# Performance work log

Hardware: AMD Instinct MI355X
Metric: run time of the kernel (lower is better)

The kernel has to match this reference:

```python
import jax, jax.numpy as jnp
import numpy as np

B, T, F, D, K, C, O = 256, 16, 8, 32, 64, 1024, 2

def setup_inputs():
    ks = jax.random.split(jax.random.key(0), 16)
    return {
        "tdata": jax.random.normal(ks[0], (B, T, F, D), jnp.float32),
        "f_mask": jax.random.randint(ks[1], (B, T, F), 0, 2, jnp.int32),
        "centers": jax.random.normal(ks[2], (F, K, D), jnp.float32),
        "pat": jax.random.randint(ks[3], (F, C, F), 0, K + 2, jnp.int32),
        "pat_rep": jax.random.normal(ks[4], (F, C, D), jnp.float32),
        "pos_cnt": jax.random.uniform(ks[5], (F, C), jnp.float32),
        "neg_cnt": jax.random.uniform(ks[6], (F, C), jnp.float32),
        "W_q": jax.random.normal(ks[7], (F, D, D), jnp.float32) * 0.1,
        "b_q": jax.random.normal(ks[8], (F, D), jnp.float32) * 0.1,
        "W_k": jax.random.normal(ks[9], (F, D, D + 1), jnp.float32) * 0.1,
        "b_k": jax.random.normal(ks[10], (F, D), jnp.float32) * 0.1,
        "W_v": jax.random.normal(ks[11], (F, D + 1, D + 1), jnp.float32) * 0.1,
        "b_v": jax.random.normal(ks[12], (F, D + 1), jnp.float32) * 0.1,
        "W_pred": jax.random.normal(ks[13], (O, F * (D + 1)), jnp.float32) * 0.1,
    }

def reference(tdata, f_mask, centers, pat, pat_rep, pos_cnt, neg_cnt,
              W_q, b_q, W_k, b_k, W_v, b_v, W_pred):
    Bv, Tv, Fv, Dv = tdata.shape
    BT = Bv * Tv
    fdata = tdata.reshape(BT, Fv, Dv)                     # [BT, F, D]

    # --- VQ nearest-centroid codes per feature (compute_codes) ---
    def codes_one(x, cen):                                # x [BT, D], cen [K, D]
        d = (jnp.sum(x * x, 1, keepdims=True)
             - 2.0 * (x @ cen.T)
             + jnp.sum(cen * cen, 1)[None, :])
        return jnp.argmin(d, axis=1)
    codes = jax.vmap(codes_one, in_axes=(1, 0), out_axes=1)(fdata, centers)  # [BT, F]
    mflat = f_mask.reshape(BT, Fv)
    # scatter_add equivalent: masked positions get code+2, unmasked get 1
    f_codes = jnp.where(mflat != 0, codes.astype(jnp.int32) + 2, 1)          # [BT, F]

    ratio = pos_cnt / (pos_cnt + neg_cnt + 1e-6)          # [F, C]
    rep = jnp.concatenate([pat_rep, ratio[..., None]], axis=-1)  # [F, C, D+1]
    query = tdata[:, -1]                                  # [B, F, D]

    def per_feature(pat_i, rep_i, q_i, Wq, bq, Wk, bk, Wv, bv):
        # pattern match: wildcard (0) always matches, else code must equal
        wild = pat_i == 0                                 # [C, F]
        eq = jnp.where(wild[None], True, f_codes[:, None, :] == pat_i[None])  # [BT, C, F]
        match = jnp.any(jnp.all(eq, axis=2).reshape(Bv, Tv, -1), axis=1)      # [B, C]
        key_t = match[..., None].astype(rep_i.dtype) * rep_i[None]            # [B, C, D+1]
        iq = q_i @ Wq.T + bq                              # [B, D]
        ik = key_t @ Wk.T + bk                            # [B, C, D]
        iv = key_t @ Wv.T + bv                            # [B, C, D+1]
        e = jnp.einsum('bcd,bd->bc', ik, iq)
        e = e - (1.0 - match.astype(e.dtype)) * 1e7
        a = jax.nn.softmax(e, axis=-1)
        v = jnp.einsum('bc,bcd->bd', a, iv)               # [B, D+1]
        return v, a

    v_all, a_all = jax.vmap(per_feature, in_axes=(0, 0, 1, 0, 0, 0, 0, 0, 0))(
        pat, rep, query, W_q, b_q, W_k, b_k, W_v, b_v)    # [F,B,D+1], [F,B,C]
    srep = jnp.swapaxes(v_all, 0, 1)                      # [B, F, D+1]
    fm = jnp.any(f_mask != 0, axis=1).astype(srep.dtype)  # [B, F]
    srep = srep * fm[..., None]
    cali = srep.reshape(Bv, -1) @ W_pred.T                # [B, O]
    return cali, a_all, srep
```

## Files before the change

### kernel.cpp

```cpp
#include <hip/hip_runtime.h>
#include <math.h>

#define Bv 256
#define Tv 16
#define Fv 8
#define Dv 32
#define Kv 64
#define Cv 1024
#define Ov 2
#define D1 33
#define CSTRIDE 33

typedef unsigned long long u64;
typedef unsigned char u8;

struct SM {
  float cen[4 * Kv * CSTRIDE];
  float xsh[Tv * Fv * Dv];
  u64   cds[Tv];
  int   fmask[Tv * Fv];
  int   fm_arr[Fv];
  int   anyf[Fv][4];
  float srep_all[Fv * D1];
  float iqs[Dv], zs[D1 + 1], vsum[D1];
  float redm[4], reds[4];
};

__device__ __forceinline__ void codes_pass(SM& sm, int pass,
    const float* __restrict__ centers) {
  int tid = threadIdx.x;
  int w = tid >> 6, lane = tid & 63;
  const float4* src = (const float4*)(centers + pass * 4 * Kv * Dv);
  #pragma unroll
  for (int it = 0; it < 8; it++) {
    int g4 = tid + it * 256;
    float4 v = src[g4];
    int g = g4 * 4;
    int row = g >> 5, col = g & 31;
    float* dst = &sm.cen[row * CSTRIDE + col];
    dst[0] = v.x; dst[1] = v.y; dst[2] = v.z; dst[3] = v.w;
  }
  __syncthreads();
  int ff = pass * 4 + w;
  float crow[Dv];
  float cc = 0.f;
  const float* rowp = &sm.cen[(w * Kv + lane) * CSTRIDE];
  #pragma unroll
  for (int j = 0; j < Dv; j++) { float cv = rowp[j]; crow[j] = cv; cc += cv * cv; }
  for (int t = 0; t < Tv; t++) {
    const float4* xp = (const float4*)&sm.xsh[(t * Fv + ff) * Dv];
    float dot = 0.f;
    #pragma unroll
    for (int i = 0; i < 8; i++) {
      float4 xv = xp[i];
      dot += crow[i*4+0]*xv.x + crow[i*4+1]*xv.y + crow[i*4+2]*xv.z + crow[i*4+3]*xv.w;
    }
    float bd = cc - 2.0f * dot;
    int bk = lane;
    #pragma unroll
    for (int off = 32; off >= 1; off >>= 1) {
      float od = __shfl_xor(bd, off, 64);
      int ok = __shfl_xor(bk, off, 64);
      if (od < bd || (od == bd && ok < bk)) { bd = od; bk = ok; }
    }
    if (lane == 0) {
      int m = sm.fmask[t * Fv + ff];
      ((u8*)sm.cds)[t * Fv + ff] = (u8)(m != 0 ? bk + 2 : 1);
    }
  }
  __syncthreads();
}

__global__ __launch_bounds__(256) void fused(
    const float* __restrict__ tdata, const int* __restrict__ f_mask,
    const float* __restrict__ centers, const int* __restrict__ pat,
    const float* __restrict__ pat_rep, const float* __restrict__ pos_cnt,
    const float* __restrict__ neg_cnt,
    const float* __restrict__ W_q, const float* __restrict__ b_q,
    const float* __restrict__ W_k, const float* __restrict__ b_k,
    const float* __restrict__ W_v, const float* __restrict__ b_v,
    const float* __restrict__ W_pred,
    float* __restrict__ cali, float* __restrict__ a_out,
    float* __restrict__ srep_out) {
  __shared__ SM sm;
  int b = blockIdx.x, tid = threadIdx.x;

  {
    const float4* src = (const float4*)(tdata + (size_t)b * (Tv * Fv * Dv));
    float4* dst = (float4*)sm.xsh;
    #pragma unroll
    for (int it = 0; it < 4; it++) dst[tid + it * 256] = src[tid + it * 256];
    if (tid < Tv * Fv) sm.fmask[tid] = f_mask[b * (Tv * Fv) + tid];
  }
  codes_pass(sm, 0, centers);
  if (tid < Fv) {
    int a = 0;
    #pragma unroll
    for (int t = 0; t < Tv; t++) a |= sm.fmask[t * Fv + tid];
    sm.fm_arr[tid] = (a != 0);
  }
  codes_pass(sm, 1, centers);

  u64 creg[Tv];
  #pragma unroll
  for (int t = 0; t < Tv; t++) creg[t] = sm.cds[t];

  for (int f = 0; f < Fv; f++) {
    u64 pp[4], cm[4];
    bool mt[4];
    #pragma unroll
    for (int jj = 0; jj < 4; jj++) {
      int c = tid + (jj << 8);
      const int4* pr = (const int4*)(pat + ((size_t)f * Cv + c) * Fv);
      int4 pa = pr[0], pb = pr[1];
      int vals[8] = {pa.x, pa.y, pa.z, pa.w, pb.x, pb.y, pb.z, pb.w};
      u64 P = 0, M = 0;
      #pragma unroll
      for (int k = 0; k < 8; k++) {
        P |= ((u64)(vals[k] & 0xFF)) << (8 * k);
        if (vals[k] != 0) M |= 0xFFull << (8 * k);
      }
      pp[jj] = P; cm[jj] = M;
      bool m = false;
      #pragma unroll
      for (int t = 0; t < Tv; t++) m = m || (((creg[t] ^ P) & M) == 0ull);
      mt[jj] = m;
    }
    bool lany = mt[0] || mt[1] || mt[2] || mt[3];
    bool wv = __any((int)lany);
    if ((tid & 63) == 0) sm.anyf[f][tid >> 6] = wv ? 1 : 0;
    __syncthreads();
    bool anym = (sm.anyf[f][0] | sm.anyf[f][1] | sm.anyf[f][2] | sm.anyf[f][3]) != 0;
    bool fm = sm.fm_arr[f] != 0;
    float* arow = a_out + (size_t)(f * Bv + b) * Cv;

    if (!anym) {
      const float uu = 1.0f / 1024.0f;
      #pragma unroll
      for (int jj = 0; jj < 4; jj++) arow[tid + (jj << 8)] = uu;
      if (tid < D1) {
        float vd = fm ? b_v[f * D1 + tid] : 0.f;
        sm.srep_all[f * D1 + tid] = vd;
        srep_out[(b * Fv + f) * D1 + tid] = vd;
      }
      continue;
    }

    if (tid < D1) sm.vsum[tid] = 0.f;
    __syncthreads();
    if (tid < Dv) {
      const float* xq = &sm.xsh[((Tv - 1) * Fv + f) * Dv];
      const float* wq = W_q + (f * Dv + tid) * Dv;
      float s = b_q[f * Dv + tid];
      #pragma unroll
      for (int j = 0; j < Dv; j++) s += wq[j] * xq[j];
      sm.iqs[tid] = s;
    }
    __syncthreads();
    if (tid < D1) {
      float s = 0.f;
      #pragma unroll
      for (int i = 0; i < Dv; i++) s += W_k[(f * Dv + i) * D1 + tid] * sm.iqs[i];
      sm.zs[tid] = s;
    }
    if (tid == D1) {
      float s = 0.f;
      #pragma unroll
      for (int i = 0; i < Dv; i++) s += b_k[f * Dv + i] * sm.iqs[i];
      sm.zs[D1] = s;
    }
    __syncthreads();

    float ev[4];
    float lmax = -INFINITY;
    #pragma unroll
    for (int jj = 0; jj < 4; jj++) {
      ev[jj] = 0.f;
      if (mt[jj]) {
        int c = tid + (jj << 8);
        const float* rp = pat_rep + (size_t)(f * Cv + c) * Dv;
        float p = pos_cnt[f * Cv + c], n = neg_cnt[f * Cv + c];
        float r = p / (p + n + 1e-6f);
        float s = sm.zs[D1] + r * sm.zs[Dv];
        for (int j = 0; j < Dv; j++) s += rp[j] * sm.zs[j];
        ev[jj] = s;
        lmax = fmaxf(lmax, s);
      }
    }
    float mx = lmax;
    #pragma unroll
    for (int off = 32; off >= 1; off >>= 1) mx = fmaxf(mx, __shfl_xor(mx, off, 64));
    if ((tid & 63) == 0) sm.redm[tid >> 6] = mx;
    __syncthreads();
    float bmax = fmaxf(fmaxf(sm.redm[0], sm.redm[1]), fmaxf(sm.redm[2], sm.redm[3]));

    float av[4] = {0.f, 0.f, 0.f, 0.f};
    float ls = 0.f;
    #pragma unroll
    for (int jj = 0; jj < 4; jj++) {
      if (mt[jj]) { av[jj] = expf(ev[jj] - bmax); ls += av[jj]; }
    }
    float ss = ls;
    #pragma unroll
    for (int off = 32; off >= 1; off >>= 1) ss += __shfl_xor(ss, off, 64);
    if ((tid & 63) == 0) sm.reds[tid >> 6] = ss;
    __syncthreads();
    float Z = sm.reds[0] + sm.reds[1] + sm.reds[2] + sm.reds[3];

    #pragma unroll
    for (int jj = 0; jj < 4; jj++) {
      float a = av[jj] / Z;
      arow[tid + (jj << 8)] = a;
      if (mt[jj] && av[jj] != 0.f) {
        int c = tid + (jj << 8);
        const float* rp = pat_rep + (size_t)(f * Cv + c) * Dv;
        float p = pos_cnt[f * Cv + c], n = neg_cnt[f * Cv + c];
        float r = p / (p + n + 1e-6f);
        for (int j = 0; j < Dv; j++) atomicAdd(&sm.vsum[j], a * rp[j]);
        atomicAdd(&sm.vsum[Dv], a * r);
      }
    }
    __syncthreads();
    float vreg = 0.f;
    if (tid < D1) {
      float s = b_v[f * D1 + tid];
      const float* wvp = W_v + (f * D1 + tid) * D1;
      for (int j = 0; j < D1; j++) s += wvp[j] * sm.vsum[j];
      vreg = s;
    }
    __syncthreads();
    if (tid < D1) {
      float vd = fm ? vreg : 0.f;
      sm.srep_all[f * D1 + tid] = vd;
      srep_out[(b * Fv + f) * D1 + tid] = vd;
    }
  }

  __syncthreads();
  if (tid < 64) {
    int o = tid >> 5, l = tid & 31;
    const float* wp = W_pred + o * (Fv * D1);
    float acc = 0.f;
    for (int i = l; i < Fv * D1; i += 32) acc += sm.srep_all[i] * wp[i];
    #pragma unroll
    for (int off = 16; off >= 1; off >>= 1) acc += __shfl_xor(acc, off, 64);
    if (l == 0) cali[b * Ov + o] = acc;
  }
}

extern "C" void kernel_launch(void* const* d_in, const int* in_sizes, int n_in,
                              void* d_out, int out_size, void* d_ws, size_t ws_size,
                              hipStream_t stream) {
  const float* tdata   = (const float*)d_in[0];
  const int*   f_mask  = (const int*)d_in[1];
  const float* centers = (const float*)d_in[2];
  const int*   pat     = (const int*)d_in[3];
  const float* pat_rep = (const float*)d_in[4];
  const float* pos_cnt = (const float*)d_in[5];
  const float* neg_cnt = (const float*)d_in[6];
  const float* W_q     = (const float*)d_in[7];
  const float* b_q     = (const float*)d_in[8];
  const float* W_k     = (const float*)d_in[9];
  const float* b_k     = (const float*)d_in[10];
  const float* W_v     = (const float*)d_in[11];
  const float* b_v     = (const float*)d_in[12];
  const float* W_pred  = (const float*)d_in[13];

  float* out = (float*)d_out;
  float* cali = out;
  float* a_all = out + (Bv * Ov);
  float* srep = out + (Bv * Ov) + (Fv * (size_t)Bv * Cv);

  fused<<<Bv, 256, 0, stream>>>(
      tdata, f_mask, centers, pat, pat_rep, pos_cnt, neg_cnt,
      W_q, b_q, W_k, b_k, W_v, b_v, W_pred,
      cali, a_all, srep);
}
```

Before: 124.6 us.

## Assign one wavefront per feature with 512 threads, removing block-wide barriers

```diff
diff --git a/kernel.cpp b/kernel.cpp
--- a/kernel.cpp
+++ b/kernel.cpp
@@ -9,69 +9,19 @@
 #define Cv 1024
 #define Ov 2
 #define D1 33
-#define CSTRIDE 33
 
 typedef unsigned long long u64;
 typedef unsigned char u8;
 
 struct SM {
-  float cen[4 * Kv * CSTRIDE];
   float xsh[Tv * Fv * Dv];
   u64   cds[Tv];
   int   fmask[Tv * Fv];
-  int   fm_arr[Fv];
-  int   anyf[Fv][4];
   float srep_all[Fv * D1];
-  float iqs[Dv], zs[D1 + 1], vsum[D1];
-  float redm[4], reds[4];
+  float vsum[Fv][D1];
 };
 
-__device__ __forceinline__ void codes_pass(SM& sm, int pass,
-    const float* __restrict__ centers) {
-  int tid = threadIdx.x;
-  int w = tid >> 6, lane = tid & 63;
-  const float4* src = (const float4*)(centers + pass * 4 * Kv * Dv);
-  #pragma unroll
-  for (int it = 0; it < 8; it++) {
-    int g4 = tid + it * 256;
-    float4 v = src[g4];
-    int g = g4 * 4;
-    int row = g >> 5, col = g & 31;
-    float* dst = &sm.cen[row * CSTRIDE + col];
-    dst[0] = v.x; dst[1] = v.y; dst[2] = v.z; dst[3] = v.w;
-  }
-  __syncthreads();
-  int ff = pass * 4 + w;
-  float crow[Dv];
-  float cc = 0.f;
-  const float* rowp = &sm.cen[(w * Kv + lane) * CSTRIDE];
-  #pragma unroll
-  for (int j = 0; j < Dv; j++) { float cv = rowp[j]; crow[j] = cv; cc += cv * cv; }
-  for (int t = 0; t < Tv; t++) {
-    const float4* xp = (const float4*)&sm.xsh[(t * Fv + ff) * Dv];
-    float dot = 0.f;
-    #pragma unroll
-    for (int i = 0; i < 8; i++) {
-      float4 xv = xp[i];
-      dot += crow[i*4+0]*xv.x + crow[i*4+1]*xv.y + crow[i*4+2]*xv.z + crow[i*4+3]*xv.w;
-    }
-    float bd = cc - 2.0f * dot;
-    int bk = lane;
-    #pragma unroll
-    for (int off = 32; off >= 1; off >>= 1) {
-      float od = __shfl_xor(bd, off, 64);
-      int ok = __shfl_xor(bk, off, 64);
-      if (od < bd || (od == bd && ok < bk)) { bd = od; bk = ok; }
-    }
-    if (lane == 0) {
-      int m = sm.fmask[t * Fv + ff];
-      ((u8*)sm.cds)[t * Fv + ff] = (u8)(m != 0 ? bk + 2 : 1);
-    }
-  }
-  __syncthreads();
-}
-
-__global__ __launch_bounds__(256) void fused(
+__global__ __launch_bounds__(512) void fused(
     const float* __restrict__ tdata, const int* __restrict__ f_mask,
     const float* __restrict__ centers, const int* __restrict__ pat,
     const float* __restrict__ pat_rep, const float* __restrict__ pos_cnt,
@@ -84,155 +34,161 @@
     float* __restrict__ srep_out) {
   __shared__ SM sm;
   int b = blockIdx.x, tid = threadIdx.x;
+  int w = tid >> 6, lane = tid & 63;
 
   {
     const float4* src = (const float4*)(tdata + (size_t)b * (Tv * Fv * Dv));
     float4* dst = (float4*)sm.xsh;
-    #pragma unroll
-    for (int it = 0; it < 4; it++) dst[tid + it * 256] = src[tid + it * 256];
+    dst[tid] = src[tid];
+    dst[tid + 512] = src[tid + 512];
     if (tid < Tv * Fv) sm.fmask[tid] = f_mask[b * (Tv * Fv) + tid];
   }
-  codes_pass(sm, 0, centers);
-  if (tid < Fv) {
-    int a = 0;
-    #pragma unroll
-    for (int t = 0; t < Tv; t++) a |= sm.fmask[t * Fv + tid];
-    sm.fm_arr[tid] = (a != 0);
-  }
-  codes_pass(sm, 1, centers);
-
+  __syncthreads();
+
+  {
+    const float4* cp = (const float4*)(centers + (size_t)(w * Kv + lane) * Dv);
+    float4 c4[8];
+    float cc = 0.f;
+    #pragma unroll
+    for (int i = 0; i < 8; i++) {
+      float4 v = cp[i];
+      c4[i] = v;
+      cc += v.x * v.x + v.y * v.y + v.z * v.z + v.w * v.w;
+    }
+    #pragma unroll
+    for (int t = 0; t < Tv; t += 2) {
+      const float4* x0 = (const float4*)&sm.xsh[(t * Fv + w) * Dv];
+      const float4* x1 = (const float4*)&sm.xsh[((t + 1) * Fv + w) * Dv];
+      float dot0 = 0.f, dot1 = 0.f;
+      #pragma unroll
+      for (int i = 0; i < 8; i++) {
+        float4 a = x0[i], bq = x1[i];
+        dot0 += c4[i].x * a.x + c4[i].y * a.y + c4[i].z * a.z + c4[i].w * a.w;
+        dot1 += c4[i].x * bq.x + c4[i].y * bq.y + c4[i].z * bq.z + c4[i].w * bq.w;
+      }
+      float d0 = cc - 2.0f * dot0;
+      float d1 = cc - 2.0f * dot1;
+      float m0 = d0, m1 = d1;
+      #pragma unroll
+      for (int off = 1; off <= 32; off <<= 1) {
+        m0 = fminf(m0, __shfl_xor(m0, off, 64));
+        m1 = fminf(m1, __shfl_xor(m1, off, 64));
+      }
+      u64 bl0 = __ballot(d0 == m0);
+      u64 bl1 = __ballot(d1 == m1);
+      int k0 = __ffsll(bl0) - 1;
+      int k1 = __ffsll(bl1) - 1;
+      if (lane == 0) {
+        ((u8*)sm.cds)[t * Fv + w] = sm.fmask[t * Fv + w] ? (u8)(k0 + 2) : (u8)1;
+        ((u8*)sm.cds)[(t + 1) * Fv + w] = sm.fmask[(t + 1) * Fv + w] ? (u8)(k1 + 2) : (u8)1;
+      }
+    }
+  }
+  __syncthreads();
+
+  int f = w;
   u64 creg[Tv];
   #pragma unroll
   for (int t = 0; t < Tv; t++) creg[t] = sm.cds[t];
 
-  for (int f = 0; f < Fv; f++) {
-    u64 pp[4], cm[4];
-    bool mt[4];
-    #pragma unroll
-    for (int jj = 0; jj < 4; jj++) {
-      int c = tid + (jj << 8);
-      const int4* pr = (const int4*)(pat + ((size_t)f * Cv + c) * Fv);
-      int4 pa = pr[0], pb = pr[1];
-      int vals[8] = {pa.x, pa.y, pa.z, pa.w, pb.x, pb.y, pb.z, pb.w};
-      u64 P = 0, M = 0;
-      #pragma unroll
-      for (int k = 0; k < 8; k++) {
-        P |= ((u64)(vals[k] & 0xFF)) << (8 * k);
-        if (vals[k] != 0) M |= 0xFFull << (8 * k);
-      }
-      pp[jj] = P; cm[jj] = M;
-      bool m = false;
-      #pragma unroll
-      for (int t = 0; t < Tv; t++) m = m || (((creg[t] ^ P) & M) == 0ull);
-      mt[jj] = m;
-    }
-    bool lany = mt[0] || mt[1] || mt[2] || mt[3];
-    bool wv = __any((int)lany);
-    if ((tid & 63) == 0) sm.anyf[f][tid >> 6] = wv ? 1 : 0;
-    __syncthreads();
-    bool anym = (sm.anyf[f][0] | sm.anyf[f][1] | sm.anyf[f][2] | sm.anyf[f][3]) != 0;
-    bool fm = sm.fm_arr[f] != 0;
-    float* arow = a_out + (size_t)(f * Bv + b) * Cv;
-
-    if (!anym) {
-      const float uu = 1.0f / 1024.0f;
-      #pragma unroll
-      for (int jj = 0; jj < 4; jj++) arow[tid + (jj << 8)] = uu;
-      if (tid < D1) {
-        float vd = fm ? b_v[f * D1 + tid] : 0.f;
-        sm.srep_all[f * D1 + tid] = vd;
-        srep_out[(b * Fv + f) * D1 + tid] = vd;
-      }
-      continue;
-    }
-
-    if (tid < D1) sm.vsum[tid] = 0.f;
-    __syncthreads();
-    if (tid < Dv) {
+  int fmlv = (lane < Tv) ? sm.fmask[lane * Fv + f] : 0;
+  bool fm = __any(fmlv != 0);
+
+  unsigned mask16 = 0u;
+  #pragma unroll 4
+  for (int jj = 0; jj < 16; jj++) {
+    int c = (jj << 6) + lane;
+    const int4* pr = (const int4*)(pat + ((size_t)f * Cv + c) * Fv);
+    int4 pa = pr[0], pb = pr[1];
+    int vals[8] = {pa.x, pa.y, pa.z, pa.w, pb.x, pb.y, pb.z, pb.w};
+    u64 P = 0, M = 0;
+    #pragma unroll
+    for (int k = 0; k < 8; k++) {
+      P |= ((u64)(vals[k] & 0xFF)) << (8 * k);
+      if (vals[k] != 0) M |= 0xFFull << (8 * k);
+    }
+    u64 pm = P & M;
+    bool m = false;
+    #pragma unroll
+    for (int t = 0; t < Tv; t++) m = m || ((creg[t] & M) == pm);
+    if (m) mask16 |= (1u << jj);
+  }
+  bool anym = __any(mask16 != 0u);
+
+  float* arow = a_out + (size_t)(f * Bv + b) * Cv;
+
+  if (!anym) {
+    const float uu = 1.0f / 1024.0f;
+    #pragma unroll
+    for (int jj = 0; jj < 16; jj++) arow[(jj << 6) + lane] = uu;
+    if (lane < D1) {
+      float vd = fm ? b_v[f * D1 + lane] : 0.f;
+      srep_out[(b * Fv + f) * D1 + lane] = vd;
+      sm.srep_all[f * D1 + lane] = vd;
+    }
+  } else {
+    if (lane < D1) sm.vsum[f][lane] = 0.f;
+    float iqv = 0.f;
+    if (lane < Dv) {
+      const float* wq = W_q + (f * Dv + lane) * Dv;
       const float* xq = &sm.xsh[((Tv - 1) * Fv + f) * Dv];
-      const float* wq = W_q + (f * Dv + tid) * Dv;
-      float s = b_q[f * Dv + tid];
-      #pragma unroll
+      float s = b_q[f * Dv + lane];
       for (int j = 0; j < Dv; j++) s += wq[j] * xq[j];
-      sm.iqs[tid] = s;
-    }
-    __syncthreads();
-    if (tid < D1) {
-      float s = 0.f;
-      #pragma unroll
-      for (int i = 0; i < Dv; i++) s += W_k[(f * Dv + i) * D1 + tid] * sm.iqs[i];
-      sm.zs[tid] = s;
-    }
-    if (tid == D1) {
-      float s = 0.f;
-      #pragma unroll
-      for (int i = 0; i < Dv; i++) s += b_k[f * Dv + i] * sm.iqs[i];
-      sm.zs[D1] = s;
-    }
-    __syncthreads();
-
-    float ev[4];
+      iqv = s;
+    }
+    float zv = 0.f;
+    for (int i = 0; i < Dv; i++) {
+      float iqi = __shfl(iqv, i, 64);
+      float coef = 0.f;
+      if (lane < D1) coef = W_k[(f * Dv + i) * D1 + lane];
+      else if (lane == D1) coef = b_k[f * Dv + i];
+      zv += coef * iqi;
+    }
+    float ev[16];
     float lmax = -INFINITY;
-    #pragma unroll
-    for (int jj = 0; jj < 4; jj++) {
+    for (int jj = 0; jj < 16; jj++) {
       ev[jj] = 0.f;
-      if (mt[jj]) {
-        int c = tid + (jj << 8);
-        const float* rp = pat_rep + (size_t)(f * Cv + c) * Dv;
+      if (mask16 & (1u << jj)) {
+        int c = (jj << 6) + lane;
+        const float* rp = pat_rep + ((size_t)f * Cv + c) * Dv;
         float p = pos_cnt[f * Cv + c], n = neg_cnt[f * Cv + c];
         float r = p / (p + n + 1e-6f);
-        float s = sm.zs[D1] + r * sm.zs[Dv];
-        for (int j = 0; j < Dv; j++) s += rp[j] * sm.zs[j];
+        float s = __shfl(zv, D1, 64) + r * __shfl(zv, Dv, 64);
+        for (int j = 0; j < Dv; j++) s += rp[j] * __shfl(zv, j, 64);
         ev[jj] = s;
         lmax = fmaxf(lmax, s);
       }
     }
-    float mx = lmax;
-    #pragma unroll
-    for (int off = 32; off >= 1; off >>= 1) mx = fmaxf(mx, __shfl_xor(mx, off, 64));
-    if ((tid & 63) == 0) sm.redm[tid >> 6] = mx;
-    __syncthreads();
-    float bmax = fmaxf(fmaxf(sm.redm[0], sm.redm[1]), fmaxf(sm.redm[2], sm.redm[3]));
-
-    float av[4] = {0.f, 0.f, 0.f, 0.f};
+    float bm = lmax;
+    #pragma unroll
+    for (int off = 1; off <= 32; off <<= 1) bm = fmaxf(bm, __shfl_xor(bm, off, 64));
     float ls = 0.f;
-    #pragma unroll
-    for (int jj = 0; jj < 4; jj++) {
-      if (mt[jj]) { av[jj] = expf(ev[jj] - bmax); ls += av[jj]; }
-    }
-    float ss = ls;
-    #pragma unroll
-    for (int off = 32; off >= 1; off >>= 1) ss += __shfl_xor(ss, off, 64);
-    if ((tid & 63) == 0) sm.reds[tid >> 6] = ss;
-    __syncthreads();
-    float Z = sm.reds[0] + sm.reds[1] + sm.reds[2] + sm.reds[3];
-
-    #pragma unroll
-    for (int jj = 0; jj < 4; jj++) {
-      float a = av[jj] / Z;
-      arow[tid + (jj << 8)] = a;
-      if (mt[jj] && av[jj] != 0.f) {
-        int c = tid + (jj << 8);
-        const float* rp = pat_rep + (size_t)(f * Cv + c) * Dv;
+    for (int jj = 0; jj < 16; jj++) {
+      if (mask16 & (1u << jj)) { ev[jj] = expf(ev[jj] - bm); ls += ev[jj]; }
+    }
+    float Zs = ls;
+    #pragma unroll
+    for (int off = 1; off <= 32; off <<= 1) Zs += __shfl_xor(Zs, off, 64);
+    for (int jj = 0; jj < 16; jj++) {
+      int c = (jj << 6) + lane;
+      bool hit = (mask16 & (1u << jj)) != 0u;
+      float a = hit ? ev[jj] / Zs : 0.f;
+      arow[c] = a;
+      if (hit && a != 0.f) {
+        const float* rp = pat_rep + ((size_t)f * Cv + c) * Dv;
         float p = pos_cnt[f * Cv + c], n = neg_cnt[f * Cv + c];
         float r = p / (p + n + 1e-6f);
-        for (int j = 0; j < Dv; j++) atomicAdd(&sm.vsum[j], a * rp[j]);
-        atomicAdd(&sm.vsum[Dv], a * r);
-      }
-    }
-    __syncthreads();
-    float vreg = 0.f;
-    if (tid < D1) {
-      float s = b_v[f * D1 + tid];
-      const float* wvp = W_v + (f * D1 + tid) * D1;
-      for (int j = 0; j < D1; j++) s += wvp[j] * sm.vsum[j];
-      vreg = s;
-    }
-    __syncthreads();
-    if (tid < D1) {
-      float vd = fm ? vreg : 0.f;
-      sm.srep_all[f * D1 + tid] = vd;
-      srep_out[(b * Fv + f) * D1 + tid] = vd;
+        for (int j = 0; j < Dv; j++) atomicAdd(&sm.vsum[f][j], a * rp[j]);
+        atomicAdd(&sm.vsum[f][Dv], a * r);
+      }
+    }
+    if (lane < D1) {
+      float s = b_v[f * D1 + lane];
+      const float* wvp = W_v + (f * D1 + lane) * D1;
+      for (int j = 0; j < D1; j++) s += wvp[j] * sm.vsum[f][j];
+      float vd = fm ? s : 0.f;
+      srep_out[(b * Fv + f) * D1 + lane] = vd;
+      sm.srep_all[f * D1 + lane] = vd;
     }
   }
 
@@ -271,7 +227,7 @@
   float* a_all = out + (Bv * Ov);
   float* srep = out + (Bv * Ov) + (Fv * (size_t)Bv * Cv);
 
-  fused<<<Bv, 256, 0, stream>>>(
+  fused<<<Bv, 512, 0, stream>>>(
       tdata, f_mask, centers, pat, pat_rep, pos_cnt, neg_cnt,
       W_q, b_q, W_k, b_k, W_v, b_v, W_pred,
       cali, a_all, srep);
```

After: 101.7 us. 1.23x faster.
